# Kernel optimization log

Hardware: AMD Instinct MI355X
Metric: run time of the kernel (lower is better)

## Reference

```python
import jax, jax.numpy as jnp
import numpy as np

N_ITEMS = 512
N_SAMPLES = 32768
WINDOW = 512
CHUNK = WINDOW // 2 + 1          # 257 rfft bins
N_COEFFS = CHUNK * 3             # 771: [mags | phases | start mags]
STEP = WINDOW // 2               # 256 hop
N_FRAMES = N_SAMPLES // STEP     # 128
BASE_RES = 0.5
SPAN = 1.0 - BASE_RES
EPS = 1e-12

_HANN = jnp.asarray(np.hanning(WINDOW), dtype=jnp.float32)


def setup_inputs() -> dict:
    key = jax.random.key(0)
    k1, k2, k3 = jax.random.split(key, 3)
    selections = jax.random.normal(k1, (8, 16, 4, N_ITEMS), dtype=jnp.float32)
    # init(x): uniform(-6, 6) * bernoulli(p=0.01)  -> sparse large-magnitude coeffs
    vals = jax.random.uniform(k2, (N_ITEMS, N_COEFFS), minval=-6.0, maxval=6.0, dtype=jnp.float32)
    mask = (jax.random.uniform(k3, (N_ITEMS, N_COEFFS)) < 0.01).astype(jnp.float32)
    items = vals * mask
    return {"selections": selections, "items": items}


def _resonance_synth(coeffs):
    # coeffs: (B, E, X, N_COEFFS)
    mags = BASE_RES + jax.nn.sigmoid(coeffs[..., :CHUNK]) * 0.9999 * SPAN       # decay per frame, in (0.5, 1)
    phases = jnp.tanh(coeffs[..., CHUNK:2 * CHUNK]) * jnp.pi                    # per-frame phase advance
    starts = jax.nn.sigmoid(coeffs[..., 2 * CHUNK:])                            # initial bin magnitudes

    # log-space cumulative decay scan across frames: mag at frame t = mags ** (t+1)
    t = jnp.arange(1, N_FRAMES + 1, dtype=jnp.float32)                          # (F,)
    log_m = jnp.log(mags + EPS)                                                 # (B,E,X,C)
    decay = jnp.exp(log_m[..., None, :] * t[:, None])                           # (B,E,X,F,C)
    phi = phases[..., None, :] * t[:, None]                                     # cumulative phase rotation

    spec = (starts[..., None, :] * decay).astype(jnp.complex64) * jnp.exp(1j * phi.astype(jnp.complex64))
    frames = jnp.fft.irfft(spec, n=WINDOW, axis=-1).astype(jnp.float32)         # (B,E,X,F,W)
    frames = frames * _HANN

    first = frames[..., :STEP]                                                  # (B,E,X,F,STEP)
    second = frames[..., STEP:]
    shifted = jnp.concatenate([jnp.zeros_like(second[..., :1, :]), second[..., :-1, :]], axis=-2)
    out = first + shifted                                                       # (B,E,X,F,STEP)
    return out.reshape(*frames.shape[:-2], N_FRAMES * STEP)                     # (B,E,X,N_SAMPLES)


def reference(selections, items):
    # select_items with selection_type='relu': non-negative mixture over the item table
    selected = jnp.einsum('bexi,ic->bexc', jax.nn.relu(selections), items)      # (B,E,X,N_COEFFS)
    res = _resonance_synth(selected)                                            # (B,E,X,N_SAMPLES)
    norm = jnp.linalg.norm(res, axis=-1, keepdims=True)
    return res / (norm + 1e-8)                                                  # unit_norm along samples
```

## Files before the change

kernel.cpp:

```cpp
#include <hip/hip_runtime.h>
#include <math.h>

#define N_ROWS   512
#define NBINS    257
#define N_COEFFS 771
#define STEP     256
#define N_FRAMES 128
#define N_SAMP   32768
#define KDIM     544
#define NCHUNK   17
#define TWO_PI   6.283185307179586f

typedef _Float16 half8 __attribute__((ext_vector_type(8)));
typedef float floatx4 __attribute__((ext_vector_type(4)));

__global__ __launch_bounds__(320) void k_params(const float* __restrict__ sel,
                                                const float* __restrict__ items,
                                                float4* __restrict__ pa,
                                                float2* __restrict__ pb) {
    int rp  = blockIdx.x;
    int t   = threadIdx.x;
    __shared__ float s[1024];
    for (int i = t; i < 1024; i += 320) {
        int rr = i >> 9, j = i & 511;
        float v = sel[(rp * 2 + rr) * 512 + j];
        s[i] = v > 0.f ? v : 0.f;
    }
    __syncthreads();
    if (t < NBINS) {
        int k = t;
        float cm0 = 0.f, cp0 = 0.f, cs0 = 0.f;
        float cm1 = 0.f, cp1 = 0.f, cs1 = 0.f;
        #pragma unroll 8
        for (int i = 0; i < 512; ++i) {
            const float* ip = items + i * N_COEFFS + k;
            float i0 = ip[0], i1 = ip[257], i2 = ip[514];
            float s0 = s[i], s1 = s[512 + i];
            cm0 = fmaf(s0, i0, cm0);  cm1 = fmaf(s1, i0, cm1);
            cp0 = fmaf(s0, i1, cp0);  cp1 = fmaf(s1, i1, cp1);
            cs0 = fmaf(s0, i2, cs0);  cs1 = fmaf(s1, i2, cs1);
        }
        float w = (k == 0 || k == 256) ? (1.f / 512.f) : (2.f / 512.f);
        #pragma unroll
        for (int rr = 0; rr < 2; ++rr) {
            float cm = rr ? cm1 : cm0, cp = rr ? cp1 : cp0, cs = rr ? cs1 : cs0;
            float sig_m = 1.f / (1.f + expf(-cm));
            float mag   = 0.5f + sig_m * 0.9999f * 0.5f;
            float lm    = logf(mag + 1e-12f);
            float ph    = tanhf(cp) * 3.14159265358979323846f;
            float sph, cph;
            sincosf(ph, &sph, &cph);
            float st = 1.f / (1.f + expf(-cs));
            int idx = (rp * 2 + rr) * NBINS + k;
            pa[idx] = make_float4(lm, ph, cph, sph);
            pb[idx] = make_float2(st * w, mag);
        }
    }
}

__global__ __launch_bounds__(256) void k_basis(_Float16* __restrict__ Bt) {
    int jg = blockIdx.x;
    int n  = ((jg >> 7) << 6) + (jg & 63) + (((jg >> 6) & 1) << 8);
    int tid = threadIdx.x;
    for (int k = tid; k < KDIM; k += 256) {
        float v;
        if (k < NBINS) {
            int r = (k * n) & 511;
            v = cosf(TWO_PI * (float)r * (1.f / 512.f));
        } else if (k < 2 * NBINS) {
            int kp = k - NBINS;
            int r = (kp * n) & 511;
            v = -sinf(TWO_PI * (float)r * (1.f / 512.f));
        } else {
            v = 0.f;
        }
        Bt[(size_t)jg * KDIM + k] = (_Float16)v;
    }
}

__global__ __launch_bounds__(512, 2) void k_row(const float4* __restrict__ pa,
                                                const float2* __restrict__ pb,
                                                const _Float16* __restrict__ basis,
                                                float* __restrict__ out) {
    __shared__ _Float16 Asm[NCHUNK * 128 * 32];
    __shared__ _Float16 Bsm[2][128 * 32];
    __shared__ float    SBB[7][64];
    __shared__ float    red[8];

    const int row  = blockIdx.x;
    const int t    = threadIdx.x;
    const int lane = t & 63;
    const int w    = t >> 6;
    const int quad = lane >> 4;
    const int l16  = lane & 15;
    const int j    = t >> 2;
    const int q    = t & 3;

    const size_t bstride = KDIM;
    half8 L0 = *(const half8*)(basis + (size_t)j * bstride + 0 * 32 + q * 8);
    half8 nxt = *(const half8*)(basis + (size_t)j * bstride + 1 * 32 + q * 8);

    {
        half8 z = {};
        *(half8*)&Asm[16 * 4096 + t * 8] = z;
    }
    __syncthreads();

    if (t < NBINS) {
        float4 P = pa[row * NBINS + t];
        float2 Q = pb[row * NBINS + t];
        float D = 512.f * Q.x * Q.y;
        float c = P.z, s = P.w;
        int k1 = t, k2 = NBINS + t;
        int c1 = k1 >> 5, g1 = (k1 & 31) >> 3, o1 = k1 & 7;
        int c2 = k2 >> 5, g2 = (k2 & 31) >> 3, o2 = k2 & 7;
        for (int f = 0; f < N_FRAMES; ++f) {
            int sw = f & 3;
            Asm[c1 * 4096 + f * 32 + ((g1 ^ sw) << 3) + o1] = (_Float16)(D * c);
            Asm[c2 * 4096 + f * 32 + ((g2 ^ sw) << 3) + o2] = (_Float16)(D * s);
            D *= Q.y;
            float nc = fmaf(c, P.z, -s * P.w);
            float ns = fmaf(s, P.z,  c * P.w);
            c = nc; s = ns;
        }
    }
    *(half8*)&Bsm[0][j * 32 + ((q ^ (j & 3)) << 3)] = L0;
    __syncthreads();

    int p = 0;
    int lcb = 0, lks = 2;
    const int m = w * 16 + l16;
    const int aswz = ((quad ^ (m & 3)) << 3);
    float oreg[4][4][4];
    float ssq = 0.f;

    #pragma unroll
    for (int cb = 0; cb < 4; ++cb) {
        floatx4 acc[8] = {};
        for (int ks = 0; ks < NCHUNK; ++ks) {
            half8 cur = nxt;
            if (lcb < 4) {
                nxt = *(const half8*)(basis + (size_t)(lcb * 128 + j) * bstride + lks * 32 + q * 8);
                if (++lks == NCHUNK) { lks = 0; ++lcb; }
            }
            if (!(cb == 3 && ks == NCHUNK - 1)) {
                *(half8*)&Bsm[p ^ 1][j * 32 + ((q ^ (j & 3)) << 3)] = cur;
            }
            half8 av = *(const half8*)&Asm[ks * 4096 + m * 32 + aswz];
            #pragma unroll
            for (int nt = 0; nt < 8; ++nt) {
                int u = nt * 16 + l16;
                half8 bv = *(const half8*)&Bsm[p][u * 32 + ((quad ^ (u & 3)) << 3)];
                acc[nt] = __builtin_amdgcn_mfma_f32_16x16x32_f16(av, bv, acc[nt], 0, 0, 0);
            }
            __syncthreads();
            p ^= 1;
        }

        float W2r[4][4];
        #pragma unroll
        for (int nt = 0; nt < 4; ++nt) {
            int n2 = 256 + cb * 64 + nt * 16 + l16;
            float h2 = 0.5f - 0.5f * cosf(TWO_PI * (float)n2 / 511.f);
            #pragma unroll
            for (int rr = 0; rr < 4; ++rr) W2r[nt][rr] = acc[nt + 4][rr] * h2;
        }
        if (quad == 3 && w < 7) {
            #pragma unroll
            for (int nt = 0; nt < 4; ++nt) SBB[w][nt * 16 + l16] = W2r[nt][3];
        }
        __syncthreads();
        #pragma unroll
        for (int nt = 0; nt < 4; ++nt) {
            int r0 = nt * 16 + l16;
            int n1 = cb * 64 + r0;
            float h1 = 0.5f - 0.5f * cosf(TWO_PI * (float)n1 / 511.f);
            float prev3 = __shfl(W2r[nt][3], (lane + 48) & 63, 64);
            float sbv = SBB[w > 0 ? w - 1 : 0][r0];
            float sec0 = (quad > 0) ? prev3 : ((w > 0) ? sbv : 0.f);
            float v0 = fmaf(acc[nt][0], h1, sec0);
            oreg[cb][nt][0] = v0; ssq = fmaf(v0, v0, ssq);
            #pragma unroll
            for (int rr = 1; rr < 4; ++rr) {
                float v = fmaf(acc[nt][rr], h1, W2r[nt][rr - 1]);
                oreg[cb][nt][rr] = v; ssq = fmaf(v, v, ssq);
            }
        }
    }

    #pragma unroll
    for (int off = 32; off > 0; off >>= 1) ssq += __shfl_down(ssq, off, 64);
    if (lane == 0) red[w] = ssq;
    __syncthreads();
    float tot = red[0] + red[1] + red[2] + red[3] + red[4] + red[5] + red[6] + red[7];
    float scale = 1.f / (sqrtf(tot) + 1e-8f);

    float* orow = out + (size_t)row * N_SAMP;
    #pragma unroll
    for (int cb = 0; cb < 4; ++cb) {
        #pragma unroll
        for (int nt = 0; nt < 4; ++nt) {
            int c = cb * 64 + nt * 16 + l16;
            #pragma unroll
            for (int rr = 0; rr < 4; ++rr) {
                int f = w * 16 + quad * 4 + rr;
                orow[f * 256 + c] = oreg[cb][nt][rr] * scale;
            }
        }
    }
}

extern "C" void kernel_launch(void* const* d_in, const int* in_sizes, int n_in,
                              void* d_out, int out_size, void* d_ws, size_t ws_size,
                              hipStream_t stream) {
    const float* sel   = (const float*)d_in[0];
    const float* items = (const float*)d_in[1];
    float* out = (float*)d_out;

    char* ws = (char*)d_ws;
    size_t off = 0;
    float4* pa   = (float4*)(ws + off); off += (size_t)N_ROWS * NBINS * 16;   off = (off + 255) & ~255ull;
    float2* pb   = (float2*)(ws + off); off += (size_t)N_ROWS * NBINS * 8;    off = (off + 255) & ~255ull;
    _Float16* basis = (_Float16*)(ws + off);

    k_params<<<dim3(N_ROWS / 2), dim3(320), 0, stream>>>(sel, items, pa, pb);
    k_basis<<<dim3(512), dim3(256), 0, stream>>>(basis);
    k_row<<<dim3(N_ROWS), dim3(512), 0, stream>>>(pa, pb, basis, out);
}
```

Baseline: 189.6 us.

## Merge prep kernels and retile row GEMM into a 2x4 warp grid over the full output

Merges the params and basis kernels into one launch and changes k_params to one row per block instead of two. The row kernel computes the whole 128x512 output tile in one pass with a 2x4 warp grid (4x8 MFMA tiles per warp). This replaces four column passes that each reloaded the full basis, cutting global basis traffic and improving A-fragment reuse. The A spectrum is generated in two phases to fit shared memory, K is padded to 576, and the basis is stored in a pre-swizzled layout. The cost is many more accumulator registers (128 floats per thread), which may hurt occupancy or cause spills under launch_bounds(512,2).

```diff
diff --git a/kernel.cpp b/kernel.cpp
--- a/kernel.cpp
+++ b/kernel.cpp
@@ -7,43 +7,40 @@
 #define STEP     256
 #define N_FRAMES 128
 #define N_SAMP   32768
-#define KDIM     544
-#define NCHUNK   17
+#define KDIM     576
+#define NCHUNK   18
+#define PCH      9
+#define PCOLS    288
 #define TWO_PI   6.283185307179586f
 
 typedef _Float16 half8 __attribute__((ext_vector_type(8)));
 typedef float floatx4 __attribute__((ext_vector_type(4)));
 
-__global__ __launch_bounds__(320) void k_params(const float* __restrict__ sel,
-                                                const float* __restrict__ items,
-                                                float4* __restrict__ pa,
-                                                float2* __restrict__ pb) {
-    int rp  = blockIdx.x;
-    int t   = threadIdx.x;
-    __shared__ float s[1024];
-    for (int i = t; i < 1024; i += 320) {
-        int rr = i >> 9, j = i & 511;
-        float v = sel[(rp * 2 + rr) * 512 + j];
-        s[i] = v > 0.f ? v : 0.f;
-    }
-    __syncthreads();
-    if (t < NBINS) {
-        int k = t;
-        float cm0 = 0.f, cp0 = 0.f, cs0 = 0.f;
-        float cm1 = 0.f, cp1 = 0.f, cs1 = 0.f;
-        #pragma unroll 8
-        for (int i = 0; i < 512; ++i) {
-            const float* ip = items + i * N_COEFFS + k;
-            float i0 = ip[0], i1 = ip[257], i2 = ip[514];
-            float s0 = s[i], s1 = s[512 + i];
-            cm0 = fmaf(s0, i0, cm0);  cm1 = fmaf(s1, i0, cm1);
-            cp0 = fmaf(s0, i1, cp0);  cp1 = fmaf(s1, i1, cp1);
-            cs0 = fmaf(s0, i2, cs0);  cs1 = fmaf(s1, i2, cs1);
-        }
-        float w = (k == 0 || k == 256) ? (1.f / 512.f) : (2.f / 512.f);
-        #pragma unroll
-        for (int rr = 0; rr < 2; ++rr) {
-            float cm = rr ? cm1 : cm0, cp = rr ? cp1 : cp0, cs = rr ? cs1 : cs0;
+__global__ __launch_bounds__(256) void k_prep(const float* __restrict__ sel,
+                                              const float* __restrict__ items,
+                                              float4* __restrict__ pa,
+                                              float2* __restrict__ pb,
+                                              _Float16* __restrict__ Bt) {
+    int bid = blockIdx.x;
+    int tid = threadIdx.x;
+    if (bid < N_ROWS) {
+        int row = bid;
+        __shared__ float s[512];
+        float v0 = sel[row * 512 + tid];
+        float v1 = sel[row * 512 + tid + 256];
+        s[tid]       = v0 > 0.f ? v0 : 0.f;
+        s[tid + 256] = v1 > 0.f ? v1 : 0.f;
+        __syncthreads();
+        for (int k = tid; k < NBINS; k += 256) {
+            float cm = 0.f, cp = 0.f, cs = 0.f;
+            #pragma unroll 8
+            for (int i = 0; i < 512; ++i) {
+                float sv = s[i];
+                const float* ip = items + i * N_COEFFS + k;
+                cm = fmaf(sv, ip[0],   cm);
+                cp = fmaf(sv, ip[257], cp);
+                cs = fmaf(sv, ip[514], cs);
+            }
             float sig_m = 1.f / (1.f + expf(-cm));
             float mag   = 0.5f + sig_m * 0.9999f * 0.5f;
             float lm    = logf(mag + 1e-12f);
@@ -51,30 +48,26 @@
             float sph, cph;
             sincosf(ph, &sph, &cph);
             float st = 1.f / (1.f + expf(-cs));
-            int idx = (rp * 2 + rr) * NBINS + k;
+            float w  = (k == 0 || k == 256) ? (1.f / 512.f) : (2.f / 512.f);
+            int idx = row * NBINS + k;
             pa[idx] = make_float4(lm, ph, cph, sph);
             pb[idx] = make_float2(st * w, mag);
         }
-    }
-}
-
-__global__ __launch_bounds__(256) void k_basis(_Float16* __restrict__ Bt) {
-    int jg = blockIdx.x;
-    int n  = ((jg >> 7) << 6) + (jg & 63) + (((jg >> 6) & 1) << 8);
-    int tid = threadIdx.x;
-    for (int k = tid; k < KDIM; k += 256) {
-        float v;
-        if (k < NBINS) {
-            int r = (k * n) & 511;
-            v = cosf(TWO_PI * (float)r * (1.f / 512.f));
-        } else if (k < 2 * NBINS) {
-            int kp = k - NBINS;
-            int r = (kp * n) & 511;
-            v = -sinf(TWO_PI * (float)r * (1.f / 512.f));
-        } else {
-            v = 0.f;
-        }
-        Bt[(size_t)jg * KDIM + k] = (_Float16)v;
+    } else {
+        int jg = bid - N_ROWS;
+        int n  = ((jg >> 7) << 6) + (jg & 63) + (((jg >> 6) & 1) << 8);
+        for (int k = tid; k < KDIM; k += 256) {
+            float v = 0.f;
+            if (k < NBINS) {
+                int r = (k * n) & 511;
+                v = cosf(TWO_PI * (float)r * (1.f / 512.f));
+            } else if (k < 2 * NBINS) {
+                int r = ((k - NBINS) * n) & 511;
+                v = -sinf(TWO_PI * (float)r * (1.f / 512.f));
+            }
+            size_t pos = ((size_t)((k >> 5) * 4 + ((k >> 3) & 3)) * 512 + jg) * 8 + (k & 7);
+            Bt[pos] = (_Float16)v;
+        }
     }
 }
 
@@ -82,109 +75,130 @@
                                                 const float2* __restrict__ pb,
                                                 const _Float16* __restrict__ basis,
                                                 float* __restrict__ out) {
-    __shared__ _Float16 Asm[NCHUNK * 128 * 32];
-    __shared__ _Float16 Bsm[2][128 * 32];
-    __shared__ float    SBB[7][64];
+    __shared__ _Float16 Asm[PCH * 4096];
+    __shared__ _Float16 Bsm[2][16384];
+    __shared__ float    SBB[4][64];
     __shared__ float    red[8];
 
     const int row  = blockIdx.x;
     const int t    = threadIdx.x;
     const int lane = t & 63;
     const int w    = t >> 6;
+    const int wm   = w >> 2;
+    const int wn   = w & 3;
     const int quad = lane >> 4;
     const int l16  = lane & 15;
-    const int j    = t >> 2;
-    const int q    = t & 3;
-
-    const size_t bstride = KDIM;
-    half8 L0 = *(const half8*)(basis + (size_t)j * bstride + 0 * 32 + q * 8);
-    half8 nxt = *(const half8*)(basis + (size_t)j * bstride + 1 * 32 + q * 8);
-
-    {
-        half8 z = {};
-        *(half8*)&Asm[16 * 4096 + t * 8] = z;
-    }
+
+    auto agen = [&](int ph) {
+        if (t < PCOLS) {
+            int gc = ph * PCOLS + t;
+            int bin; bool isCos;
+            if (gc < NBINS)          { bin = gc;          isCos = true;  }
+            else if (gc < 2 * NBINS) { bin = gc - NBINS;  isCos = false; }
+            else                     { bin = 0;           isCos = true;  }
+            float4 P = pa[row * NBINS + bin];
+            float2 Q = pb[row * NBINS + bin];
+            float D = 512.f * Q.x * Q.y;
+            if (gc >= 2 * NBINS) D = 0.f;
+            float c = P.z, s = P.w;
+            int ch = t >> 5, g = (t >> 3) & 3, o = t & 7;
+            _Float16* base = &Asm[ch * 4096 + o];
+            for (int f = 0; f < N_FRAMES; ++f) {
+                float val = isCos ? D * c : D * s;
+                base[f * 32 + ((g ^ ((f >> 1) & 3) ^ ((f >> 3) & 3)) << 3)] = (_Float16)val;
+                D *= Q.y;
+                float nc = fmaf(c, P.z, -s * P.w);
+                float ns = fmaf(s, P.z,  c * P.w);
+                c = nc; s = ns;
+            }
+        }
+    };
+
+    half8 L[4];
+    #pragma unroll
+    for (int g = 0; g < 4; ++g)
+        L[g] = *(const half8*)(basis + ((size_t)(0 * 4 + g) * 512 + t) * 8);
+    agen(0);
+    #pragma unroll
+    for (int g = 0; g < 4; ++g)
+        *(half8*)&Bsm[0][g * 4096 + t * 8] = L[g];
+    #pragma unroll
+    for (int g = 0; g < 4; ++g)
+        L[g] = *(const half8*)(basis + ((size_t)(1 * 4 + g) * 512 + t) * 8);
     __syncthreads();
 
-    if (t < NBINS) {
-        float4 P = pa[row * NBINS + t];
-        float2 Q = pb[row * NBINS + t];
-        float D = 512.f * Q.x * Q.y;
-        float c = P.z, s = P.w;
-        int k1 = t, k2 = NBINS + t;
-        int c1 = k1 >> 5, g1 = (k1 & 31) >> 3, o1 = k1 & 7;
-        int c2 = k2 >> 5, g2 = (k2 & 31) >> 3, o2 = k2 & 7;
-        for (int f = 0; f < N_FRAMES; ++f) {
-            int sw = f & 3;
-            Asm[c1 * 4096 + f * 32 + ((g1 ^ sw) << 3) + o1] = (_Float16)(D * c);
-            Asm[c2 * 4096 + f * 32 + ((g2 ^ sw) << 3) + o2] = (_Float16)(D * s);
-            D *= Q.y;
-            float nc = fmaf(c, P.z, -s * P.w);
-            float ns = fmaf(s, P.z,  c * P.w);
-            c = nc; s = ns;
-        }
-    }
-    *(half8*)&Bsm[0][j * 32 + ((q ^ (j & 3)) << 3)] = L0;
-    __syncthreads();
-
+    floatx4 acc[4][8] = {};
     int p = 0;
-    int lcb = 0, lks = 2;
-    const int m = w * 16 + l16;
-    const int aswz = ((quad ^ (m & 3)) << 3);
-    float oreg[4][4][4];
-    float ssq = 0.f;
-
-    #pragma unroll
-    for (int cb = 0; cb < 4; ++cb) {
-        floatx4 acc[8] = {};
-        for (int ks = 0; ks < NCHUNK; ++ks) {
-            half8 cur = nxt;
-            if (lcb < 4) {
-                nxt = *(const half8*)(basis + (size_t)(lcb * 128 + j) * bstride + lks * 32 + q * 8);
-                if (++lks == NCHUNK) { lks = 0; ++lcb; }
-            }
-            if (!(cb == 3 && ks == NCHUNK - 1)) {
-                *(half8*)&Bsm[p ^ 1][j * 32 + ((q ^ (j & 3)) << 3)] = cur;
-            }
-            half8 av = *(const half8*)&Asm[ks * 4096 + m * 32 + aswz];
+    for (int ph = 0; ph < 2; ++ph) {
+        if (ph == 1) { agen(1); __syncthreads(); }
+        for (int ks = 0; ks < PCH; ++ks) {
+            int gc = ph * PCH + ks;
+            if (gc < NCHUNK - 1) {
+                #pragma unroll
+                for (int g = 0; g < 4; ++g)
+                    *(half8*)&Bsm[p ^ 1][g * 4096 + t * 8] = L[g];
+                if (gc < NCHUNK - 2) {
+                    #pragma unroll
+                    for (int g = 0; g < 4; ++g)
+                        L[g] = *(const half8*)(basis + ((size_t)((gc + 2) * 4 + g) * 512 + t) * 8);
+                }
+            }
+            half8 av[4];
+            #pragma unroll
+            for (int mt = 0; mt < 4; ++mt) {
+                int m = wm * 64 + mt * 16 + l16;
+                av[mt] = *(const half8*)&Asm[ks * 4096 + m * 32 +
+                          ((quad ^ ((m >> 1) & 3) ^ ((m >> 3) & 3)) << 3)];
+            }
             #pragma unroll
             for (int nt = 0; nt < 8; ++nt) {
-                int u = nt * 16 + l16;
-                half8 bv = *(const half8*)&Bsm[p][u * 32 + ((quad ^ (u & 3)) << 3)];
-                acc[nt] = __builtin_amdgcn_mfma_f32_16x16x32_f16(av, bv, acc[nt], 0, 0, 0);
+                int u = wn * 128 + nt * 16 + l16;
+                half8 bv = *(const half8*)&Bsm[p][quad * 4096 + u * 8];
+                #pragma unroll
+                for (int mt = 0; mt < 4; ++mt)
+                    acc[mt][nt] = __builtin_amdgcn_mfma_f32_16x16x32_f16(av[mt], bv, acc[mt][nt], 0, 0, 0);
             }
             __syncthreads();
             p ^= 1;
         }
-
-        float W2r[4][4];
+    }
+
+    float h1[4], h2[4];
+    #pragma unroll
+    for (int nt = 0; nt < 4; ++nt) {
+        int n1 = wn * 64 + nt * 16 + l16;
+        h1[nt] = 0.5f - 0.5f * cosf(TWO_PI * (float)n1 / 511.f);
+        h2[nt] = 0.5f - 0.5f * cosf(TWO_PI * (float)(n1 + 256) / 511.f);
+    }
+    if (wm == 0 && quad == 3) {
+        #pragma unroll
+        for (int nt = 0; nt < 4; ++nt)
+            SBB[wn][nt * 16 + l16] = acc[3][nt + 4][3] * h2[nt];
+    }
+    __syncthreads();
+
+    float oreg[4][4][4];
+    float prevLast[4] = {0.f, 0.f, 0.f, 0.f};
+    float ssq = 0.f;
+    #pragma unroll
+    for (int mt = 0; mt < 4; ++mt) {
         #pragma unroll
         for (int nt = 0; nt < 4; ++nt) {
-            int n2 = 256 + cb * 64 + nt * 16 + l16;
-            float h2 = 0.5f - 0.5f * cosf(TWO_PI * (float)n2 / 511.f);
-            #pragma unroll
-            for (int rr = 0; rr < 4; ++rr) W2r[nt][rr] = acc[nt + 4][rr] * h2;
-        }
-        if (quad == 3 && w < 7) {
-            #pragma unroll
-            for (int nt = 0; nt < 4; ++nt) SBB[w][nt * 16 + l16] = W2r[nt][3];
-        }
-        __syncthreads();
-        #pragma unroll
-        for (int nt = 0; nt < 4; ++nt) {
-            int r0 = nt * 16 + l16;
-            int n1 = cb * 64 + r0;
-            float h1 = 0.5f - 0.5f * cosf(TWO_PI * (float)n1 / 511.f);
-            float prev3 = __shfl(W2r[nt][3], (lane + 48) & 63, 64);
-            float sbv = SBB[w > 0 ? w - 1 : 0][r0];
-            float sec0 = (quad > 0) ? prev3 : ((w > 0) ? sbv : 0.f);
-            float v0 = fmaf(acc[nt][0], h1, sec0);
-            oreg[cb][nt][0] = v0; ssq = fmaf(v0, v0, ssq);
+            float W2[4];
+            #pragma unroll
+            for (int rr = 0; rr < 4; ++rr) W2[rr] = acc[mt][nt + 4][rr] * h2[nt];
+            float tmp = (quad == 3) ? prevLast[nt] : W2[3];
+            float carry = __shfl(tmp, (lane + 48) & 63, 64);
+            if (mt == 0 && quad == 0)
+                carry = (wm == 1) ? SBB[wn][nt * 16 + l16] : 0.f;
+            float v = fmaf(acc[mt][nt][0], h1[nt], carry);
+            oreg[mt][nt][0] = v; ssq = fmaf(v, v, ssq);
             #pragma unroll
             for (int rr = 1; rr < 4; ++rr) {
-                float v = fmaf(acc[nt][rr], h1, W2r[nt][rr - 1]);
-                oreg[cb][nt][rr] = v; ssq = fmaf(v, v, ssq);
-            }
+                v = fmaf(acc[mt][nt][rr], h1[nt], W2[rr - 1]);
+                oreg[mt][nt][rr] = v; ssq = fmaf(v, v, ssq);
+            }
+            prevLast[nt] = W2[3];
         }
     }
 
@@ -197,14 +211,14 @@
 
     float* orow = out + (size_t)row * N_SAMP;
     #pragma unroll
-    for (int cb = 0; cb < 4; ++cb) {
+    for (int mt = 0; mt < 4; ++mt) {
         #pragma unroll
         for (int nt = 0; nt < 4; ++nt) {
-            int c = cb * 64 + nt * 16 + l16;
+            int n1 = wn * 64 + nt * 16 + l16;
             #pragma unroll
             for (int rr = 0; rr < 4; ++rr) {
-                int f = w * 16 + quad * 4 + rr;
-                orow[f * 256 + c] = oreg[cb][nt][rr] * scale;
+                int f = wm * 64 + mt * 16 + quad * 4 + rr;
+                orow[f * 256 + n1] = oreg[mt][nt][rr] * scale;
             }
         }
     }
@@ -223,7 +237,6 @@
     float2* pb   = (float2*)(ws + off); off += (size_t)N_ROWS * NBINS * 8;    off = (off + 255) & ~255ull;
     _Float16* basis = (_Float16*)(ws + off);
 
-    k_params<<<dim3(N_ROWS / 2), dim3(320), 0, stream>>>(sel, items, pa, pb);
-    k_basis<<<dim3(512), dim3(256), 0, stream>>>(basis);
+    k_prep<<<dim3(N_ROWS + 512), dim3(256), 0, stream>>>(sel, items, pa, pb, basis);
     k_row<<<dim3(N_ROWS), dim3(512), 0, stream>>>(pa, pb, basis, out);
 }
```

Result: faster. 182.5 us (-3.8%).
